# Optimization experiments

Hardware: AMD Instinct MI355X
Metric: run time of the kernel (lower is better)

The kernel has to match this reference:

```python
import jax, jax.numpy as jnp
import numpy as np


def _quat_to_rot(q):
    # q: [B,4] (w,x,y,z); normalize as the torch code does when norm != 1
    q = q / jnp.linalg.norm(q, axis=-1, keepdims=True)
    w, x, y, z = q[:, 0], q[:, 1], q[:, 2], q[:, 3]
    r00 = 1 - 2 * y**2 - 2 * z**2
    r01 = 2 * x * y - 2 * z * w
    r02 = 2 * x * z + 2 * y * w
    r10 = 2 * x * y + 2 * z * w
    r11 = 1 - 2 * x**2 - 2 * z**2
    r12 = 2 * y * z - 2 * x * w
    r20 = 2 * x * z - 2 * y * w
    r21 = 2 * y * z + 2 * x * w
    r22 = 1 - 2 * x**2 - 2 * y**2
    R = jnp.stack([
        jnp.stack([r00, r01, r02], axis=-1),
        jnp.stack([r10, r11, r12], axis=-1),
        jnp.stack([r20, r21, r22], axis=-1),
    ], axis=-2)  # [B,3,3]
    return R


def setup_inputs() -> dict:
    key = jax.random.key(0)
    k1, k2, k3, k4 = jax.random.split(key, 4)
    B, N = 32, 262144
    return {
        "pcd_mis": jax.random.normal(k1, (B, N, 3), dtype=jnp.float32),
        "T_mis": jax.random.normal(k2, (B, 4, 4), dtype=jnp.float32),
        "delta_q_pred": jax.random.normal(k3, (B, 4), dtype=jnp.float32),
        "delta_t_pred": jax.random.normal(k4, (B, 3), dtype=jnp.float32),
    }


def reference(pcd_mis, T_mis, delta_q_pred, delta_t_pred):
    B = delta_q_pred.shape[0]
    R = _quat_to_rot(delta_q_pred)                      # [B,3,3]
    t = delta_t_pred[:, :, None]                        # [B,3,1]
    top = jnp.concatenate([R, t], axis=-1)              # [B,3,4]
    bottom = jnp.broadcast_to(
        jnp.array([0.0, 0.0, 0.0, 1.0], dtype=pcd_mis.dtype), (B, 1, 4))
    delta_T = jnp.concatenate([top, bottom], axis=-2)   # [B,4,4]
    inv_T = jnp.linalg.inv(delta_T)                     # [B,4,4]
    batch_T_pred = jnp.einsum('bij,bjk->bik', inv_T, T_mis)  # [B,4,4]
    # homogeneous point transform: only first 3 output rows are kept
    # new = (inv_T @ [p;1])[:3] = p @ Rinv^T + tinv
    pcd_new = jnp.einsum('bij,bnj->bni', inv_T[:, :3, :3], pcd_mis) \
        + inv_T[:, None, :3, 3]                          # [B,N,3]
    return (batch_T_pred, pcd_new)
```

## Files before the change

### kernel.cpp

```cpp
#include <hip/hip_runtime.h>
#include <math.h>

struct Inv {
    float i00, i01, i02, it0;
    float i10, i11, i12, it1;
    float i20, i21, i22, it2;
};

__device__ __forceinline__ Inv make_inv(const float* __restrict__ q,
                                        const float* __restrict__ t, int b) {
    float w = q[b * 4 + 0], x = q[b * 4 + 1], y = q[b * 4 + 2], z = q[b * 4 + 3];
    float inv_n = 1.0f / sqrtf(w * w + x * x + y * y + z * z);
    w *= inv_n; x *= inv_n; y *= inv_n; z *= inv_n;
    float R00 = 1.f - 2.f * y * y - 2.f * z * z;
    float R01 = 2.f * x * y - 2.f * z * w;
    float R02 = 2.f * x * z + 2.f * y * w;
    float R10 = 2.f * x * y + 2.f * z * w;
    float R11 = 1.f - 2.f * x * x - 2.f * z * z;
    float R12 = 2.f * y * z - 2.f * x * w;
    float R20 = 2.f * x * z - 2.f * y * w;
    float R21 = 2.f * y * z + 2.f * x * w;
    float R22 = 1.f - 2.f * x * x - 2.f * y * y;
    float t0 = t[b * 3 + 0], t1 = t[b * 3 + 1], t2 = t[b * 3 + 2];
    Inv v;
    v.i00 = R00; v.i01 = R10; v.i02 = R20; v.it0 = -(R00 * t0 + R10 * t1 + R20 * t2);
    v.i10 = R01; v.i11 = R11; v.i12 = R21; v.it1 = -(R01 * t0 + R11 * t1 + R21 * t2);
    v.i20 = R02; v.i21 = R12; v.i22 = R22; v.it2 = -(R02 * t0 + R12 * t1 + R22 * t2);
    return v;
}

__device__ __forceinline__ void xf(const Inv& M, float px, float py, float pz,
                                   float& ox, float& oy, float& oz) {
    ox = fmaf(M.i00, px, fmaf(M.i01, py, fmaf(M.i02, pz, M.it0)));
    oy = fmaf(M.i10, px, fmaf(M.i11, py, fmaf(M.i12, pz, M.it1)));
    oz = fmaf(M.i20, px, fmaf(M.i21, py, fmaf(M.i22, pz, M.it2)));
}

__global__ __launch_bounds__(256) void realign_fused_kernel(
        const float4* __restrict__ pcd,
        const float* __restrict__ T_mis,
        const float* __restrict__ q,
        const float* __restrict__ t,
        float* __restrict__ out_mat,
        float4* __restrict__ out_pcd,
        int f4_per_batch) {
    __shared__ float4 smem[768];
    const int b = blockIdx.y;
    const int tid = threadIdx.x;
    const size_t chunk = (size_t)b * (size_t)f4_per_batch + (size_t)blockIdx.x * 768u;

    float4 r0 = pcd[chunk + tid];
    float4 r1 = pcd[chunk + 256 + tid];
    float4 r2 = pcd[chunk + 512 + tid];

    const Inv M = make_inv(q, t, b);

    smem[tid]       = r0;
    smem[256 + tid] = r1;
    smem[512 + tid] = r2;

    if (blockIdx.x == 0 && tid < 16) {
        const int i = tid >> 2;
        const int j = tid & 3;
        const float* Tb = T_mis + b * 16;
        float val;
        if (i < 3) {
            float a0, a1, a2, it;
            if (i == 0)      { a0 = M.i00; a1 = M.i01; a2 = M.i02; it = M.it0; }
            else if (i == 1) { a0 = M.i10; a1 = M.i11; a2 = M.i12; it = M.it1; }
            else             { a0 = M.i20; a1 = M.i21; a2 = M.i22; it = M.it2; }
            val = fmaf(a0, Tb[0 * 4 + j],
                  fmaf(a1, Tb[1 * 4 + j],
                  fmaf(a2, Tb[2 * 4 + j],
                       it * Tb[3 * 4 + j])));
        } else {
            val = Tb[3 * 4 + j];
        }
        out_mat[b * 16 + tid] = val;
    }

    __syncthreads();

    float4 v0 = smem[3 * tid + 0];
    float4 v1 = smem[3 * tid + 1];
    float4 v2 = smem[3 * tid + 2];
    float4 o0, o1, o2;
    xf(M, v0.x, v0.y, v0.z, o0.x, o0.y, o0.z);
    xf(M, v0.w, v1.x, v1.y, o0.w, o1.x, o1.y);
    xf(M, v1.z, v1.w, v2.x, o1.z, o1.w, o2.x);
    xf(M, v2.y, v2.z, v2.w, o2.y, o2.z, o2.w);
    smem[3 * tid + 0] = o0;
    smem[3 * tid + 1] = o1;
    smem[3 * tid + 2] = o2;

    __syncthreads();

    out_pcd[chunk + tid]       = smem[tid];
    out_pcd[chunk + 256 + tid] = smem[256 + tid];
    out_pcd[chunk + 512 + tid] = smem[512 + tid];
}

extern "C" void kernel_launch(void* const* d_in, const int* in_sizes, int n_in,
                              void* d_out, int out_size, void* d_ws, size_t ws_size,
                              hipStream_t stream) {
    const float* pcd   = (const float*)d_in[0];
    const float* T_mis = (const float*)d_in[1];
    const float* q     = (const float*)d_in[2];
    const float* t     = (const float*)d_in[3];
    float* out = (float*)d_out;

    const int B = in_sizes[2] / 4;
    const long long N = (long long)in_sizes[0] / (3LL * B);
    const int f4_per_batch = (int)(3 * N / 4);
    const int blocks_x = f4_per_batch / 768;

    dim3 grid(blocks_x, B);
    realign_fused_kernel<<<grid, 256, 0, stream>>>(
        (const float4*)pcd, T_mis, q, t,
        out, (float4*)(out + B * 16), f4_per_batch);
}
```

Before: 180.2 us.

## Use persistent grid-stride blocks with next-chunk prefetch and nontemporal stores

Replaces the one-block-per-chunk 2D grid with 2048 persistent blocks that loop over chunks. Each block loads the next chunk's three float4s into registers while it transforms the current chunk, so loads overlap compute and stores. Output stores become nontemporal to reduce cache pollution on this streaming write. Block 0 now computes all B 4x4 output matrices itself, and the batch index is derived from a shift, which assumes a power-of-two number of chunks per batch.

New measurement: 182.8 us. No clear change (+1.5%).

```diff
diff --git a/kernel.cpp b/kernel.cpp
--- a/kernel.cpp
+++ b/kernel.cpp
@@ -1,5 +1,7 @@
 #include <hip/hip_runtime.h>
 #include <math.h>
+
+typedef float nt_float4 __attribute__((ext_vector_type(4)));
 
 struct Inv {
     float i00, i01, i02, it0;
@@ -36,68 +38,91 @@
     oz = fmaf(M.i20, px, fmaf(M.i21, py, fmaf(M.i22, pz, M.it2)));
 }
 
-__global__ __launch_bounds__(256) void realign_fused_kernel(
+__device__ __forceinline__ void nt_store(float4 v, float4* p) {
+    nt_float4 nv = { v.x, v.y, v.z, v.w };
+    __builtin_nontemporal_store(nv, (nt_float4*)p);
+}
+
+__global__ __launch_bounds__(256) void realign_persist(
         const float4* __restrict__ pcd,
         const float* __restrict__ T_mis,
         const float* __restrict__ q,
         const float* __restrict__ t,
         float* __restrict__ out_mat,
         float4* __restrict__ out_pcd,
-        int f4_per_batch) {
+        int n_bchunks, int bcpb_shift, int B) {
     __shared__ float4 smem[768];
-    const int b = blockIdx.y;
     const int tid = threadIdx.x;
-    const size_t chunk = (size_t)b * (size_t)f4_per_batch + (size_t)blockIdx.x * 768u;
 
-    float4 r0 = pcd[chunk + tid];
-    float4 r1 = pcd[chunk + 256 + tid];
-    float4 r2 = pcd[chunk + 512 + tid];
-
-    const Inv M = make_inv(q, t, b);
-
-    smem[tid]       = r0;
-    smem[256 + tid] = r1;
-    smem[512 + tid] = r2;
-
-    if (blockIdx.x == 0 && tid < 16) {
-        const int i = tid >> 2;
-        const int j = tid & 3;
-        const float* Tb = T_mis + b * 16;
-        float val;
-        if (i < 3) {
-            float a0, a1, a2, it;
-            if (i == 0)      { a0 = M.i00; a1 = M.i01; a2 = M.i02; it = M.it0; }
-            else if (i == 1) { a0 = M.i10; a1 = M.i11; a2 = M.i12; it = M.it1; }
-            else             { a0 = M.i20; a1 = M.i21; a2 = M.i22; it = M.it2; }
-            val = fmaf(a0, Tb[0 * 4 + j],
-                  fmaf(a1, Tb[1 * 4 + j],
-                  fmaf(a2, Tb[2 * 4 + j],
-                       it * Tb[3 * 4 + j])));
-        } else {
-            val = Tb[3 * 4 + j];
+    if (blockIdx.x == 0) {
+        for (int e = tid; e < B * 16; e += blockDim.x) {
+            int b = e >> 4, i = (e >> 2) & 3, j = e & 3;
+            const float* Tb = T_mis + b * 16;
+            float val;
+            if (i < 3) {
+                Inv M = make_inv(q, t, b);
+                float a0, a1, a2, it;
+                if (i == 0)      { a0 = M.i00; a1 = M.i01; a2 = M.i02; it = M.it0; }
+                else if (i == 1) { a0 = M.i10; a1 = M.i11; a2 = M.i12; it = M.it1; }
+                else             { a0 = M.i20; a1 = M.i21; a2 = M.i22; it = M.it2; }
+                val = fmaf(a0, Tb[j], fmaf(a1, Tb[4 + j], fmaf(a2, Tb[8 + j], it * Tb[12 + j])));
+            } else {
+                val = Tb[12 + j];
+            }
+            out_mat[e] = val;
         }
-        out_mat[b * 16 + tid] = val;
     }
 
-    __syncthreads();
+    int bc = blockIdx.x;
+    size_t base = (size_t)bc * 768u;
+    float4 r0 = pcd[base + tid];
+    float4 r1 = pcd[base + 256 + tid];
+    float4 r2 = pcd[base + 512 + tid];
 
-    float4 v0 = smem[3 * tid + 0];
-    float4 v1 = smem[3 * tid + 1];
-    float4 v2 = smem[3 * tid + 2];
-    float4 o0, o1, o2;
-    xf(M, v0.x, v0.y, v0.z, o0.x, o0.y, o0.z);
-    xf(M, v0.w, v1.x, v1.y, o0.w, o1.x, o1.y);
-    xf(M, v1.z, v1.w, v2.x, o1.z, o1.w, o2.x);
-    xf(M, v2.y, v2.z, v2.w, o2.y, o2.z, o2.w);
-    smem[3 * tid + 0] = o0;
-    smem[3 * tid + 1] = o1;
-    smem[3 * tid + 2] = o2;
+    while (true) {
+        const int bcn = bc + gridDim.x;
+        const bool more = (bcn < n_bchunks);
+        float4 p0, p1, p2;
+        if (more) {
+            size_t nb = (size_t)bcn * 768u;
+            p0 = pcd[nb + tid];
+            p1 = pcd[nb + 256 + tid];
+            p2 = pcd[nb + 512 + tid];
+        }
 
-    __syncthreads();
+        const int b = bc >> bcpb_shift;
+        const Inv M = make_inv(q, t, b);
 
-    out_pcd[chunk + tid]       = smem[tid];
-    out_pcd[chunk + 256 + tid] = smem[256 + tid];
-    out_pcd[chunk + 512 + tid] = smem[512 + tid];
+        smem[tid]       = r0;
+        smem[256 + tid] = r1;
+        smem[512 + tid] = r2;
+        __syncthreads();
+
+        float4 v0 = smem[3 * tid + 0];
+        float4 v1 = smem[3 * tid + 1];
+        float4 v2 = smem[3 * tid + 2];
+        float4 o0, o1, o2;
+        xf(M, v0.x, v0.y, v0.z, o0.x, o0.y, o0.z);
+        xf(M, v0.w, v1.x, v1.y, o0.w, o1.x, o1.y);
+        xf(M, v1.z, v1.w, v2.x, o1.z, o1.w, o2.x);
+        xf(M, v2.y, v2.z, v2.w, o2.y, o2.z, o2.w);
+        smem[3 * tid + 0] = o0;
+        smem[3 * tid + 1] = o1;
+        smem[3 * tid + 2] = o2;
+        __syncthreads();
+
+        float4 s0 = smem[tid];
+        float4 s1 = smem[256 + tid];
+        float4 s2 = smem[512 + tid];
+        nt_store(s0, &out_pcd[base + tid]);
+        nt_store(s1, &out_pcd[base + 256 + tid]);
+        nt_store(s2, &out_pcd[base + 512 + tid]);
+
+        if (!more) break;
+        r0 = p0; r1 = p1; r2 = p2;
+        bc = bcn;
+        base = (size_t)bcn * 768u;
+    }
 }
 
 extern "C" void kernel_launch(void* const* d_in, const int* in_sizes, int n_in,
@@ -112,10 +137,14 @@
     const int B = in_sizes[2] / 4;
     const long long N = (long long)in_sizes[0] / (3LL * B);
     const int f4_per_batch = (int)(3 * N / 4);
-    const int blocks_x = f4_per_batch / 768;
+    const int bcpb = f4_per_batch / 768;
+    int bcpb_shift = 0;
+    while ((1 << bcpb_shift) < bcpb) bcpb_shift++;
+    const int n_bchunks = B * bcpb;
 
-    dim3 grid(blocks_x, B);
-    realign_fused_kernel<<<grid, 256, 0, stream>>>(
+    const int blocks = 2048;
+    realign_persist<<<blocks, 256, 0, stream>>>(
         (const float4*)pcd, T_mis, q, t,
-        out, (float4*)(out + B * 16), f4_per_batch);
+        out, (float4*)(out + B * 16),
+        n_bchunks, bcpb_shift, B);
 }
```
